# Kernel tuning notes

Measured on AMD Instinct MI355X. Metric: run time of the kernel, lower is better.

Reference implementation:

```python
import jax, jax.numpy as jnp
import numpy as np

SENTINEL = 1 << 20  # fill value for padded unique rows; far outside real coord range


def setup_inputs() -> dict:
    key = jax.random.key(0)
    k1, k2, k3, k4, k5, kw = jax.random.split(key, 6)
    M, C = 400000, 128
    voxel_features = jax.random.normal(k1, (M, C), dtype=jnp.float32)
    # coords: (batch_idx, z, y, x)
    b = jax.random.randint(k2, (M, 1), 0, 4, dtype=jnp.int32)
    z = jax.random.randint(k3, (M, 1), 0, 40, dtype=jnp.int32)
    y = jax.random.randint(k4, (M, 1), 0, 1024, dtype=jnp.int32)
    x = jax.random.randint(k5, (M, 1), 0, 1024, dtype=jnp.int32)
    voxel_coords = jnp.concatenate([b, z, y, x], axis=1)
    # layer-1 (stride=1) uses a random (in,out) matmul weight in the original;
    # materialize it as a fixed parameter for determinism.
    W0 = jax.random.normal(kw, (C, C), dtype=jnp.float32)
    return {"voxel_features": voxel_features, "voxel_coords": voxel_coords,
            "W0": W0, "batch_size": 4}


def _forward(voxel_features, W0, voxel_coords):
    M = voxel_features.shape[0]
    # layer 1: stride=1 -> relu then matmul (placeholder dense path)
    feats = jnp.maximum(voxel_features, 0.0) @ W0  # (M, 128)
    coords = voxel_coords
    # layers 2 and 3: stride=2 -> quantize coords (ALL 4 cols, incl. batch idx,
    # matching the original), unique, scatter-add features, relu
    for _ in range(2):
        coords = jnp.floor(coords.astype(jnp.float32) / 2.0).astype(jnp.int32)
        uniq, inv = jnp.unique(coords, axis=0, return_inverse=True,
                               size=M, fill_value=SENTINEL)
        inv = inv.reshape(-1)
        feats = jax.ops.segment_sum(feats, inv, num_segments=M)  # fused scatter-add
        feats = jnp.maximum(feats, 0.0)
        coords = uniq
    # rows beyond the true unique count are zero padding (sentinel coords)
    return feats


def reference(voxel_features, voxel_coords, W0, batch_size):
    return _forward(voxel_features, W0, voxel_coords)
```

## Files before the change

### kernel.cpp

```cpp
#include <hip/hip_runtime.h>
#include <stdint.h>

#define C 128

typedef __attribute__((ext_vector_type(8))) short bf16x8;
typedef __attribute__((ext_vector_type(4))) float f32x4;

__device__ __forceinline__ uint32_t f2bf1(float f) {
    uint32_t u = __float_as_uint(f);
    return (u + 0x7FFFu + ((u >> 16) & 1u)) >> 16;
}


__global__ __launch_bounds__(512) void zeroconv_kernel(
    uint4* __restrict__ zbase, int nquads,
    const float* __restrict__ W, ushort* __restrict__ Wt, int nzb) {
    int b = blockIdx.x, t = threadIdx.x;
    if (b < nzb) {
        int i = b * 512 + t;
        if (i < nquads) zbase[i] = (uint4){0u, 0u, 0u, 0u};
    } else {
        int id = (b - nzb) * 512 + t;
        int n = id >> 7, k = id & 127;
        Wt[id] = (ushort)f2bf1(W[k * C + n]);
    }
}

__global__ __launch_bounds__(512) void mark_kernel(
    const int* __restrict__ coords, uint32_t* __restrict__ bm1,
    uint32_t* __restrict__ bm2, int M) {
    int i = blockIdx.x * 512 + threadIdx.x;
    if (i >= M) return;
    int bb = coords[4*i+0], z = coords[4*i+1], y = coords[4*i+2], x = coords[4*i+3];
    uint32_t k1 = ((uint32_t)(bb>>1)<<23) | ((uint32_t)(z>>1)<<18) |
                  ((uint32_t)(y>>1)<<9)  | (uint32_t)(x>>1);
    uint32_t k2 = ((uint32_t)(z>>2)<<16) | ((uint32_t)(y>>2)<<8) | (uint32_t)(x>>2);
    atomicOr(&bm1[k1>>5], 1u << (k1 & 31));
    atomicOr(&bm2[k2>>5], 1u << (k2 & 31));
}

__device__ __forceinline__ void bscan1_512(const uint32_t* bm, uint32_t* bs,
                                           int blk, uint32_t* s, int t) {
    int base = blk * 1024 + t * 2;
    uint32_t sum = __popc(bm[base]) + __popc(bm[base+1]);
    s[t] = sum;
    __syncthreads();
    for (int off = 256; off > 0; off >>= 1) {
        if (t < off) s[t] += s[t + off];
        __syncthreads();
    }
    if (t == 0) bs[blk] = s[0];
}

__device__ __forceinline__ void bscan3_512(const uint32_t* bm, const uint32_t* bs,
                                           uint32_t* wp, int blk, uint32_t* s, int t) {
    int base = blk * 1024 + t * 2;
    uint32_t p0 = __popc(bm[base]), p1 = __popc(bm[base+1]);
    uint32_t sum = p0 + p1;
    s[t] = sum;
    __syncthreads();
    for (int off = 1; off < 512; off <<= 1) {
        uint32_t add = (t >= off) ? s[t - off] : 0u;
        __syncthreads();
        s[t] += add;
        __syncthreads();
    }
    uint32_t ex = s[t] - sum + bs[blk];
    wp[base]   = ex;
    wp[base+1] = ex + p0;
}

__device__ __forceinline__ void blksum_scan_512(uint32_t* bs, uint32_t* total,
                                                int nb, uint32_t* s, int t) {
    uint32_t v = (t < nb) ? bs[t] : 0u;
    s[t] = v;
    __syncthreads();
    for (int off = 1; off < 512; off <<= 1) {
        uint32_t add = (t >= off) ? s[t - off] : 0u;
        __syncthreads();
        s[t] += add;
        __syncthreads();
    }
    if (t < nb) bs[t] = s[t] - v;
    if (t == nb - 1) *total = s[t];
}

__device__ __forceinline__ void vscan1_512(const uint32_t* v, uint32_t* bs,
                                           int blk, int n, uint32_t* s, int t) {
    int base = blk * 1024 + t * 2;
    uint32_t sum = 0;
    if (base     < n) sum += v[base];
    if (base + 1 < n) sum += v[base+1];
    s[t] = sum;
    __syncthreads();
    for (int off = 256; off > 0; off >>= 1) {
        if (t < off) s[t] += s[t + off];
        __syncthreads();
    }
    if (t == 0) bs[blk] = s[0];
}

__device__ __forceinline__ void vscan3_512(const uint32_t* v, const uint32_t* bs,
                                           uint32_t* ex_out, int blk, int n,
                                           uint32_t* s, int t) {
    int base = blk * 1024 + t * 2;
    uint32_t p0 = (base     < n) ? v[base]   : 0u;
    uint32_t p1 = (base + 1 < n) ? v[base+1] : 0u;
    uint32_t sum = p0 + p1;
    s[t] = sum;
    __syncthreads();
    for (int off = 1; off < 512; off <<= 1) {
        uint32_t add = (t >= off) ? s[t - off] : 0u;
        __syncthreads();
        s[t] += add;
        __syncthreads();
    }
    uint32_t e = s[t] - sum + bs[blk];
    if (base     < n) ex_out[base]   = e;
    if (base + 1 < n) ex_out[base+1] = e + p0;
}

__global__ __launch_bounds__(512) void mscan1_kernel(
    const uint32_t* __restrict__ bm1, uint32_t* __restrict__ bs1,
    const uint32_t* __restrict__ bm2, uint32_t* __restrict__ bs2) {
    __shared__ uint32_t s[512];
    int b = blockIdx.x, t = threadIdx.x;
    if (b < 512) bscan1_512(bm1, bs1, b, s, t);
    else         bscan1_512(bm2, bs2, b - 512, s, t);
}

__global__ __launch_bounds__(512) void mscan2_kernel(
    uint32_t* __restrict__ bs1, uint32_t* __restrict__ bs2,
    uint32_t* __restrict__ totals) {
    __shared__ uint32_t s[512];
    int t = threadIdx.x;
    if (blockIdx.x == 0) blksum_scan_512(bs1, &totals[0], 512, s, t);
    else                 blksum_scan_512(bs2, &totals[1], 32,  s, t);
}

__global__ __launch_bounds__(512) void mscan3_kernel(
    const uint32_t* __restrict__ bm1, const uint32_t* __restrict__ bs1,
    uint32_t* __restrict__ wp1,
    const uint32_t* __restrict__ bm2, const uint32_t* __restrict__ bs2,
    uint32_t* __restrict__ wp2) {
    __shared__ uint32_t s[512];
    int b = blockIdx.x, t = threadIdx.x;
    if (b < 512) bscan3_512(bm1, bs1, wp1, b, s, t);
    else         bscan3_512(bm2, bs2, wp2, b - 512, s, t);
}

__global__ __launch_bounds__(512) void count_kernel(
    const int* __restrict__ coords, const uint32_t* __restrict__ bm1,
    const uint32_t* __restrict__ wp1, uint32_t* __restrict__ counts,
    uint32_t* __restrict__ rank1_arr, uint32_t* __restrict__ slot1, int M) {
    int i = blockIdx.x * 512 + threadIdx.x;
    if (i >= M) return;
    int b = coords[4*i+0], z = coords[4*i+1], y = coords[4*i+2], x = coords[4*i+3];
    uint32_t k1 = ((uint32_t)(b>>1)<<23) | ((uint32_t)(z>>1)<<18) |
                  ((uint32_t)(y>>1)<<9)  | (uint32_t)(x>>1);
    uint32_t r1 = wp1[k1>>5] + __popc(bm1[k1>>5] & ((1u << (k1 & 31)) - 1u));
    rank1_arr[i] = r1;
    slot1[i] = atomicAdd(&counts[r1], 1u);
}

__global__ __launch_bounds__(512) void mk1_kernel(
    const uint32_t* __restrict__ counts, uint32_t* __restrict__ bsc,
    const uint32_t* __restrict__ bm1, const uint32_t* __restrict__ wp1,
    const uint32_t* __restrict__ bm2, const uint32_t* __restrict__ wp2,
    uint32_t* __restrict__ parent_r2, uint32_t* __restrict__ rowcounts2,
    uint32_t* __restrict__ childbase, int M, int nbc, int nwords) {
    int b = blockIdx.x, t = threadIdx.x;
    if (b < nbc) {
        __shared__ uint32_t s[512];
        vscan1_512(counts, bsc, b, M, s, t);
        return;
    }
    int w = (b - nbc) * 512 + t;
    if (w >= nwords) return;
    uint32_t bits = bm1[w];
    if (!bits) return;
    uint32_t r1 = wp1[w];
    while (bits) {
        int bit = __ffs(bits) - 1;
        uint32_t k1 = ((uint32_t)w << 5) | (uint32_t)bit;
        uint32_t z1 = (k1 >> 18) & 31u, y1 = (k1 >> 9) & 511u, x1 = k1 & 511u;
        uint32_t k2 = ((z1 >> 1) << 16) | ((y1 >> 1) << 8) | (x1 >> 1);
        uint32_t word2 = bm2[k2 >> 5];
        uint32_t r2 = wp2[k2 >> 5] + __popc(word2 & ((1u << (k2 & 31)) - 1u));
        parent_r2[r1] = r2;
        childbase[r1] = atomicAdd(&rowcounts2[r2], counts[r1]);
        r1++;
        bits &= bits - 1;
    }
}

__global__ __launch_bounds__(512) void mk2_kernel(
    uint32_t* __restrict__ bsc, uint32_t* __restrict__ totals,
    const uint32_t* __restrict__ rowcounts2, uint32_t* __restrict__ bsc2,
    int M, int nbc) {
    __shared__ uint32_t s[512];
    int b = blockIdx.x, t = threadIdx.x;
    if (b == 0) blksum_scan_512(bsc, &totals[2], nbc, s, t);
    else        vscan1_512(rowcounts2, bsc2, b - 1, M, s, t);
}

__global__ __launch_bounds__(512) void mk3_kernel(
    const uint32_t* __restrict__ counts, const uint32_t* __restrict__ bsc,
    uint32_t* __restrict__ start1,
    uint32_t* __restrict__ bsc2, uint32_t* __restrict__ totals,
    int M, int nbc) {
    __shared__ uint32_t s[512];
    int b = blockIdx.x, t = threadIdx.x;
    if (b < nbc) vscan3_512(counts, bsc, start1, b, M, s, t);
    else         blksum_scan_512(bsc2, &totals[3], nbc, s, t);
}

__global__ __launch_bounds__(512) void mk4_kernel(
    const uint32_t* __restrict__ rank1_arr, const uint32_t* __restrict__ start1,
    const uint32_t* __restrict__ slot1, uint32_t* __restrict__ perm,
    const uint32_t* __restrict__ rowcounts2, const uint32_t* __restrict__ bsc2,
    uint32_t* __restrict__ rowstart2, int M, int npb, int nbc) {
    int b = blockIdx.x, t = threadIdx.x;
    if (b < npb) {
        int i = b * 512 + t;
        if (i >= M) return;
        uint32_t r1 = rank1_arr[i];
        perm[start1[r1] + slot1[i]] = i;
        return;
    }
    __shared__ uint32_t s[512];
    vscan3_512(rowcounts2, bsc2, rowstart2, b - npb, M, s, t);
}

__global__ __launch_bounds__(512) void flatten_kernel(
    const uint32_t* __restrict__ parent_r2, const uint32_t* __restrict__ counts,
    const uint32_t* __restrict__ start1, const uint32_t* __restrict__ rowstart2,
    const uint32_t* __restrict__ childbase, const uint32_t* __restrict__ perm,
    uint32_t* __restrict__ perm_f, const uint32_t* __restrict__ totals, int M) {
    int i = blockIdx.x * 512 + threadIdx.x;
    if (i >= M) return;
    uint32_t U1 = totals[0];
    if ((uint32_t)i >= U1) return;
    uint32_t r2 = parent_r2[i];
    uint32_t cnt = counts[i];
    uint32_t dst = rowstart2[r2] + childbase[i];
    uint32_t s = start1[i];
    perm_f[dst] = perm[s] | 0x80000000u;
    for (uint32_t q = 1; q < cnt; ++q) perm_f[dst + q] = perm[s + q];
}

__device__ __forceinline__ void gemm_loadX(const float* __restrict__ X,
                                           int tile, int lm, int kg, float4* pf) {
    const char* xb = (const char*)X + ((size_t)tile*16 + lm)*512 + kg*32;
    #pragma unroll
    for (int ks = 0; ks < 4; ++ks) {
        pf[2*ks]   = *(const float4*)(xb + ks*128);
        pf[2*ks+1] = *(const float4*)(xb + ks*128 + 16);
    }
}

__device__ __forceinline__ void gemm_compute(const float4* pf, const char* wbase,
                                             ushort* __restrict__ g, int tile,
                                             int lm, int kg) {
    bf16x8 af[4];
    #pragma unroll
    for (int ks = 0; ks < 4; ++ks) {
        float4 a = pf[2*ks], b = pf[2*ks+1];
        union { uint32_t u[4]; bf16x8 v; } cv;
        cv.u[0] = f2bf1(fmaxf(a.x,0.f)) | (f2bf1(fmaxf(a.y,0.f)) << 16);
        cv.u[1] = f2bf1(fmaxf(a.z,0.f)) | (f2bf1(fmaxf(a.w,0.f)) << 16);
        cv.u[2] = f2bf1(fmaxf(b.x,0.f)) | (f2bf1(fmaxf(b.y,0.f)) << 16);
        cv.u[3] = f2bf1(fmaxf(b.z,0.f)) | (f2bf1(fmaxf(b.w,0.f)) << 16);
        af[ks] = cv.v;
    }
    ushort* grow = g + (size_t)((size_t)tile*16 + 4*kg)*128 + lm;
    #pragma unroll
    for (int n = 0; n < 8; ++n) {
        bf16x8 b0 = *(const bf16x8*)(wbase + n*256);
        bf16x8 b1 = *(const bf16x8*)(wbase + n*256 + 8192);
        bf16x8 b2 = *(const bf16x8*)(wbase + n*256 + 16384);
        bf16x8 b3 = *(const bf16x8*)(wbase + n*256 + 24576);
        f32x4 acc = (f32x4){0.f, 0.f, 0.f, 0.f};
        acc = __builtin_amdgcn_mfma_f32_16x16x32_bf16(af[0], b0, acc, 0, 0, 0);
        acc = __builtin_amdgcn_mfma_f32_16x16x32_bf16(af[1], b1, acc, 0, 0, 0);
        acc = __builtin_amdgcn_mfma_f32_16x16x32_bf16(af[2], b2, acc, 0, 0, 0);
        acc = __builtin_amdgcn_mfma_f32_16x16x32_bf16(af[3], b3, acc, 0, 0, 0);
        #pragma unroll
        for (int r = 0; r < 4; ++r)
            grow[(size_t)r*128 + 16*n] = (ushort)f2bf1(acc[r]);
    }
}

__global__ __launch_bounds__(256) void gemm_kernel(
    const float* __restrict__ X, const ushort* __restrict__ Wt,
    ushort* __restrict__ g, int M) {
    __shared__ __align__(16) ushort wlds[16384];
    const int t = threadIdx.x;
    {
        int sm = t & 15, kc = t >> 4;
        const char* src = (const char*)Wt;
        char* dst = (char*)wlds;
        #pragma unroll
        for (int n = 0; n < 8; ++n) {
            uint4 v = *(const uint4*)(src + n*4096 + sm*256 + kc*16);
            *(uint4*)(dst + (kc>>2)*8192 + (kc&3)*2048 + n*256 + sm*16) = v;
        }
    }
    __syncthreads();
    const int l = t & 63;
    const int lm = l & 15, kg = l >> 4;
    const int ntiles = M >> 4;
    const int nw = gridDim.x * 4;
    int tile = blockIdx.x * 4 + (t >> 6);
    const char* wbase = (const char*)wlds + kg*2048 + lm*16;

    float4 pfA[8], pfB[8];
    if (tile < ntiles)      gemm_loadX(X, tile, lm, kg, pfA);
    if (tile + nw < ntiles) gemm_loadX(X, tile + nw, lm, kg, pfB);
    while (true) {
        if (tile >= ntiles) break;
        gemm_compute(pfA, wbase, g, tile, lm, kg);
        if (tile + 2*nw < ntiles) gemm_loadX(X, tile + 2*nw, lm, kg, pfA);
        tile += nw;
        if (tile >= ntiles) break;
        gemm_compute(pfB, wbase, g, tile, lm, kg);
        if (tile + 2*nw < ntiles) gemm_loadX(X, tile + 2*nw, lm, kg, pfB);
        tile += nw;
    }
}

__global__ __launch_bounds__(256) void gather2_kernel(
    const uint32_t* __restrict__ rowstart2, const uint32_t* __restrict__ rowcounts2,
    const uint32_t* __restrict__ perm_f, const ushort* __restrict__ g,
    float* __restrict__ out, int M) {
    int wid = (blockIdx.x * 256 + threadIdx.x) >> 6;
    wid = __builtin_amdgcn_readfirstlane(wid);
    int lane = threadIdx.x & 63;
    if (wid >= M) return;
    const uint32_t* G = (const uint32_t*)g;
    float accx = 0.f, accy = 0.f;
    uint32_t n = rowcounts2[wid];
    if (n) {
        uint32_t s = rowstart2[wid];
        uint32_t ev = (lane < (int)n) ? perm_f[s + lane] : 0u;
        float sx = 0.f, sy = 0.f;
        uint32_t ecur = (uint32_t)__shfl((int)ev, 0);
        uint32_t pk = G[(size_t)(ecur & 0x7FFFFFFFu) * 64 + lane];
        for (uint32_t q = 1; q < n; ++q) {
            uint32_t en = (q < 64u) ? (uint32_t)__shfl((int)ev, (int)q)
                                    : perm_f[s + q];
            uint32_t pkn = G[(size_t)(en & 0x7FFFFFFFu) * 64 + lane];
            sx += __uint_as_float(pk << 16);
            sy += __uint_as_float(pk & 0xFFFF0000u);
            if (en >> 31) {
                accx += fmaxf(sx, 0.f); accy += fmaxf(sy, 0.f);
                sx = 0.f; sy = 0.f;
            }
            pk = pkn;
        }
        sx += __uint_as_float(pk << 16);
        sy += __uint_as_float(pk & 0xFFFF0000u);
        accx += fmaxf(sx, 0.f);
        accy += fmaxf(sy, 0.f);
    }
    float2 o; o.x = accx; o.y = accy;
    ((float2*)out)[(size_t)wid * 64 + lane] = o;
}

extern "C" void kernel_launch(void* const* d_in, const int* in_sizes, int n_in,
                              void* d_out, int out_size, void* d_ws, size_t ws_size,
                              hipStream_t stream) {
    const float* X      = (const float*)d_in[0];
    const int*   coords = (const int*)d_in[1];
    const float* W      = (const float*)d_in[2];
    const int M = in_sizes[0] / C;

    const int NW1 = 1 << 19;
    const int NW2 = 1 << 15;
    const int NBC = (M + 1023) / 1024;
    const int NPB = (M + 511) / 512;

    char* ws = (char*)d_ws;
    size_t off = 0;
    ushort*   g         = (ushort*)(ws + off);   off += (size_t)M * C * 2;
    uint32_t* bm1       = (uint32_t*)(ws + off); off += (size_t)NW1 * 4;
    uint32_t* bm2       = (uint32_t*)(ws + off); off += (size_t)NW2 * 4;
    uint32_t* counts    = (uint32_t*)(ws + off); off += (size_t)M * 4;
    uint32_t* rowcounts2= (uint32_t*)(ws + off); off += (size_t)M * 4;
    const size_t zero_off   = (size_t)M * C * 2;
    const size_t zero_bytes = off - zero_off;
    uint32_t* wp1       = (uint32_t*)(ws + off); off += (size_t)NW1 * 4;
    uint32_t* wp2       = (uint32_t*)(ws + off); off += (size_t)NW2 * 4;
    uint32_t* bs1       = (uint32_t*)(ws + off); off += 512 * 4;
    uint32_t* bs2       = (uint32_t*)(ws + off); off += 512 * 4;
    uint32_t* bsc       = (uint32_t*)(ws + off); off += 512 * 4;
    uint32_t* bsc2      = (uint32_t*)(ws + off); off += 512 * 4;
    uint32_t* totals    = (uint32_t*)(ws + off); off += 4 * 4;
    uint32_t* start1    = (uint32_t*)(ws + off); off += (size_t)M * 4;
    uint32_t* rank1_arr = (uint32_t*)(ws + off); off += (size_t)M * 4;
    uint32_t* slot1     = (uint32_t*)(ws + off); off += (size_t)M * 4;
    uint32_t* perm      = (uint32_t*)(ws + off); off += (size_t)M * 4;
    uint32_t* parent_r2 = (uint32_t*)(ws + off); off += (size_t)M * 4;
    uint32_t* childbase = (uint32_t*)(ws + off); off += (size_t)M * 4;
    uint32_t* rowstart2 = (uint32_t*)(ws + off); off += (size_t)M * 4;
    ushort*   Wt        = (ushort*)(ws + off);   off += (size_t)C * C * 2;
    uint32_t* perm_f    = rank1_arr;

    const int NQ  = (int)(zero_bytes / 16);
    const int NZB = (NQ + 511) / 512;

    zeroconv_kernel<<<NZB + 32, 512, 0, stream>>>((uint4*)(ws + zero_off), NQ, W, Wt, NZB);
    mark_kernel<<<NPB, 512, 0, stream>>>(coords, bm1, bm2, M);
    mscan1_kernel<<<544, 512, 0, stream>>>(bm1, bs1, bm2, bs2);
    mscan2_kernel<<<2, 512, 0, stream>>>(bs1, bs2, totals);
    mscan3_kernel<<<544, 512, 0, stream>>>(bm1, bs1, wp1, bm2, bs2, wp2);
    count_kernel<<<NPB, 512, 0, stream>>>(coords, bm1, wp1, counts, rank1_arr, slot1, M);
    mk1_kernel<<<NBC + NW1/512, 512, 0, stream>>>(counts, bsc, bm1, wp1, bm2, wp2,
                                                  parent_r2, rowcounts2, childbase,
                                                  M, NBC, NW1);
    mk2_kernel<<<1 + NBC, 512, 0, stream>>>(bsc, totals, rowcounts2, bsc2, M, NBC);
    mk3_kernel<<<NBC + 1, 512, 0, stream>>>(counts, bsc, start1, bsc2, totals, M, NBC);
    mk4_kernel<<<NPB + NBC, 512, 0, stream>>>(rank1_arr, start1, slot1, perm,
                                              rowcounts2, bsc2, rowstart2, M, NPB, NBC);
    flatten_kernel<<<NPB, 512, 0, stream>>>(
        parent_r2, counts, start1, rowstart2, childbase, perm, perm_f, totals, M);
    gemm_kernel<<<1280, 256, 0, stream>>>(X, Wt, g, M);
    gather2_kernel<<<(M + 3) / 4, 256, 0, stream>>>(
        rowstart2, rowcounts2, perm_f, g, (float*)d_out, M);
}
```

Measured before the change: 278.7 us.

## Split dense GEMM into slices fused into each index-building kernel

Removes the standalone GEMM launch and hands contiguous tile ranges of the relu+bf16 MFMA matmul to extra blocks appended to each of the latency-bound index-building kernels (mark, scans, count, mk1-4, flatten). The small serial kernels then share the GPU with GEMM work instead of leaving it mostly idle. Several scan kernels move to 256-thread blocks handling four words per thread, and the final output uses nontemporal stores. In exchange every kernel now reserves 32KB of shared memory, which can lower occupancy for the index-building blocks, and the GEMM slice percentages are hand-tuned.

```diff
diff --git a/kernel.cpp b/kernel.cpp
--- a/kernel.cpp
+++ b/kernel.cpp
@@ -5,6 +5,7 @@
 
 typedef __attribute__((ext_vector_type(8))) short bf16x8;
 typedef __attribute__((ext_vector_type(4))) float f32x4;
+typedef __attribute__((ext_vector_type(2))) float f32x2;
 
 __device__ __forceinline__ uint32_t f2bf1(float f) {
     uint32_t u = __float_as_uint(f);
@@ -12,54 +13,103 @@
 }
 
 
-__global__ __launch_bounds__(512) void zeroconv_kernel(
-    uint4* __restrict__ zbase, int nquads,
-    const float* __restrict__ W, ushort* __restrict__ Wt, int nzb) {
-    int b = blockIdx.x, t = threadIdx.x;
-    if (b < nzb) {
-        int i = b * 512 + t;
-        if (i < nquads) zbase[i] = (uint4){0u, 0u, 0u, 0u};
-    } else {
-        int id = (b - nzb) * 512 + t;
-        int n = id >> 7, k = id & 127;
-        Wt[id] = (ushort)f2bf1(W[k * C + n]);
-    }
-}
-
-__global__ __launch_bounds__(512) void mark_kernel(
-    const int* __restrict__ coords, uint32_t* __restrict__ bm1,
-    uint32_t* __restrict__ bm2, int M) {
-    int i = blockIdx.x * 512 + threadIdx.x;
-    if (i >= M) return;
-    int bb = coords[4*i+0], z = coords[4*i+1], y = coords[4*i+2], x = coords[4*i+3];
-    uint32_t k1 = ((uint32_t)(bb>>1)<<23) | ((uint32_t)(z>>1)<<18) |
-                  ((uint32_t)(y>>1)<<9)  | (uint32_t)(x>>1);
-    uint32_t k2 = ((uint32_t)(z>>2)<<16) | ((uint32_t)(y>>2)<<8) | (uint32_t)(x>>2);
-    atomicOr(&bm1[k1>>5], 1u << (k1 & 31));
-    atomicOr(&bm2[k2>>5], 1u << (k2 & 31));
-}
-
-__device__ __forceinline__ void bscan1_512(const uint32_t* bm, uint32_t* bs,
+__device__ __forceinline__ void gemm_loadX(const float* __restrict__ X,
+                                           int tile, int lm, int kg, float4* pf) {
+    const char* xb = (const char*)X + ((size_t)tile*16 + lm)*512 + kg*32;
+    #pragma unroll
+    for (int ks = 0; ks < 4; ++ks) {
+        pf[2*ks]   = *(const float4*)(xb + ks*128);
+        pf[2*ks+1] = *(const float4*)(xb + ks*128 + 16);
+    }
+}
+
+__device__ __forceinline__ void gemm_compute(const float4* pf, const char* wbase,
+                                             ushort* __restrict__ g, int tile,
+                                             int lm, int kg) {
+    bf16x8 af[4];
+    #pragma unroll
+    for (int ks = 0; ks < 4; ++ks) {
+        float4 a = pf[2*ks], b = pf[2*ks+1];
+        union { uint32_t u[4]; bf16x8 v; } cv;
+        cv.u[0] = f2bf1(fmaxf(a.x,0.f)) | (f2bf1(fmaxf(a.y,0.f)) << 16);
+        cv.u[1] = f2bf1(fmaxf(a.z,0.f)) | (f2bf1(fmaxf(a.w,0.f)) << 16);
+        cv.u[2] = f2bf1(fmaxf(b.x,0.f)) | (f2bf1(fmaxf(b.y,0.f)) << 16);
+        cv.u[3] = f2bf1(fmaxf(b.z,0.f)) | (f2bf1(fmaxf(b.w,0.f)) << 16);
+        af[ks] = cv.v;
+    }
+    ushort* grow = g + (size_t)((size_t)tile*16 + 4*kg)*128 + lm;
+    #pragma unroll
+    for (int n = 0; n < 8; ++n) {
+        bf16x8 b0 = *(const bf16x8*)(wbase + n*256);
+        bf16x8 b1 = *(const bf16x8*)(wbase + n*256 + 8192);
+        bf16x8 b2 = *(const bf16x8*)(wbase + n*256 + 16384);
+        bf16x8 b3 = *(const bf16x8*)(wbase + n*256 + 24576);
+        f32x4 acc = (f32x4){0.f, 0.f, 0.f, 0.f};
+        acc = __builtin_amdgcn_mfma_f32_16x16x32_bf16(af[0], b0, acc, 0, 0, 0);
+        acc = __builtin_amdgcn_mfma_f32_16x16x32_bf16(af[1], b1, acc, 0, 0, 0);
+        acc = __builtin_amdgcn_mfma_f32_16x16x32_bf16(af[2], b2, acc, 0, 0, 0);
+        acc = __builtin_amdgcn_mfma_f32_16x16x32_bf16(af[3], b3, acc, 0, 0, 0);
+        #pragma unroll
+        for (int r = 0; r < 4; ++r)
+            grow[(size_t)r*128 + 16*n] = (ushort)f2bf1(acc[r]);
+    }
+}
+
+__device__ void gemm_slice(const float* __restrict__ X,
+                           const ushort* __restrict__ Wt,
+                           ushort* __restrict__ g, char* smem,
+                           int gb, int ngb, int t0, int t1) {
+    const int t = threadIdx.x;
+    const int nthreads = blockDim.x;
+    for (int q = t; q < 2048; q += nthreads) {
+        int ks = q >> 9, kg = (q >> 7) & 3, n = (q >> 4) & 7, sm = q & 15;
+        ((uint4*)smem)[q] = ((const uint4*)Wt)[n*256 + sm*16 + ks*4 + kg];
+    }
+    __syncthreads();
+    const int l = t & 63, wv = t >> 6, nwv = nthreads >> 6;
+    const int lm = l & 15, kg = l >> 4;
+    const char* wbase = smem + kg*2048 + lm*16;
+    const int stride = ngb * nwv;
+    int tile = t0 + gb * nwv + wv;
+
+    float4 pfA[8], pfB[8];
+    if (tile < t1)          gemm_loadX(X, tile, lm, kg, pfA);
+    if (tile + stride < t1) gemm_loadX(X, tile + stride, lm, kg, pfB);
+    while (true) {
+        if (tile >= t1) break;
+        gemm_compute(pfA, wbase, g, tile, lm, kg);
+        if (tile + 2*stride < t1) gemm_loadX(X, tile + 2*stride, lm, kg, pfA);
+        tile += stride;
+        if (tile >= t1) break;
+        gemm_compute(pfB, wbase, g, tile, lm, kg);
+        if (tile + 2*stride < t1) gemm_loadX(X, tile + 2*stride, lm, kg, pfB);
+        tile += stride;
+    }
+}
+
+__device__ __forceinline__ void bscan1_256(const uint32_t* bm, uint32_t* bs,
                                            int blk, uint32_t* s, int t) {
-    int base = blk * 1024 + t * 2;
-    uint32_t sum = __popc(bm[base]) + __popc(bm[base+1]);
+    int base = blk * 1024 + t * 4;
+    uint32_t sum = __popc(bm[base]) + __popc(bm[base+1]) +
+                   __popc(bm[base+2]) + __popc(bm[base+3]);
     s[t] = sum;
     __syncthreads();
-    for (int off = 256; off > 0; off >>= 1) {
+    for (int off = 128; off > 0; off >>= 1) {
         if (t < off) s[t] += s[t + off];
         __syncthreads();
     }
     if (t == 0) bs[blk] = s[0];
 }
 
-__device__ __forceinline__ void bscan3_512(const uint32_t* bm, const uint32_t* bs,
+__device__ __forceinline__ void bscan3_256(const uint32_t* bm, const uint32_t* bs,
                                            uint32_t* wp, int blk, uint32_t* s, int t) {
-    int base = blk * 1024 + t * 2;
-    uint32_t p0 = __popc(bm[base]), p1 = __popc(bm[base+1]);
-    uint32_t sum = p0 + p1;
+    int base = blk * 1024 + t * 4;
+    uint32_t p0 = __popc(bm[base]),   p1 = __popc(bm[base+1]);
+    uint32_t p2 = __popc(bm[base+2]), p3 = __popc(bm[base+3]);
+    uint32_t sum = p0 + p1 + p2 + p3;
     s[t] = sum;
     __syncthreads();
-    for (int off = 1; off < 512; off <<= 1) {
+    for (int off = 1; off < 256; off <<= 1) {
         uint32_t add = (t >= off) ? s[t - off] : 0u;
         __syncthreads();
         s[t] += add;
@@ -68,6 +118,23 @@
     uint32_t ex = s[t] - sum + bs[blk];
     wp[base]   = ex;
     wp[base+1] = ex + p0;
+    wp[base+2] = ex + p0 + p1;
+    wp[base+3] = ex + p0 + p1 + p2;
+}
+
+__device__ __forceinline__ void vscan1_256(const uint32_t* v, uint32_t* bs,
+                                           int blk, int n, uint32_t* s, int t) {
+    int base = blk * 1024 + t * 4;
+    uint32_t sum = 0;
+    #pragma unroll
+    for (int j = 0; j < 4; j++) sum += (base + j < n) ? v[base + j] : 0u;
+    s[t] = sum;
+    __syncthreads();
+    for (int off = 128; off > 0; off >>= 1) {
+        if (t < off) s[t] += s[t + off];
+        __syncthreads();
+    }
+    if (t == 0) bs[blk] = s[0];
 }
 
 __device__ __forceinline__ void blksum_scan_512(uint32_t* bs, uint32_t* total,
@@ -120,62 +187,114 @@
     if (base + 1 < n) ex_out[base+1] = e + p0;
 }
 
-__global__ __launch_bounds__(512) void mscan1_kernel(
+__global__ __launch_bounds__(256) void zeroconv_kernel(
+    uint4* __restrict__ zbase, int nquads,
+    const float* __restrict__ W, ushort* __restrict__ Wt, int nzb) {
+    int b = blockIdx.x, t = threadIdx.x;
+    if (b < nzb) {
+        int i = b * 256 + t;
+        if (i < nquads) zbase[i] = (uint4){0u, 0u, 0u, 0u};
+    } else {
+        int id = (b - nzb) * 256 + t;
+        int n = id >> 7, k = id & 127;
+        Wt[id] = (ushort)f2bf1(W[k * C + n]);
+    }
+}
+
+__global__ __launch_bounds__(256) void markg_kernel(
+    const int* __restrict__ coords, uint32_t* __restrict__ bm1,
+    uint32_t* __restrict__ bm2, int M, int nprep,
+    const float* __restrict__ X, const ushort* __restrict__ Wt,
+    ushort* __restrict__ g, int ngb, int t0, int t1) {
+    __shared__ __align__(16) char smem[32768];
+    int b = blockIdx.x;
+    if (b >= nprep) { gemm_slice(X, Wt, g, smem, b - nprep, ngb, t0, t1); return; }
+    int i = b * 256 + threadIdx.x;
+    if (i >= M) return;
+    int bb = coords[4*i+0], z = coords[4*i+1], y = coords[4*i+2], x = coords[4*i+3];
+    uint32_t k1 = ((uint32_t)(bb>>1)<<23) | ((uint32_t)(z>>1)<<18) |
+                  ((uint32_t)(y>>1)<<9)  | (uint32_t)(x>>1);
+    uint32_t k2 = ((uint32_t)(z>>2)<<16) | ((uint32_t)(y>>2)<<8) | (uint32_t)(x>>2);
+    atomicOr(&bm1[k1>>5], 1u << (k1 & 31));
+    atomicOr(&bm2[k2>>5], 1u << (k2 & 31));
+}
+
+__global__ __launch_bounds__(256) void mscan1g_kernel(
     const uint32_t* __restrict__ bm1, uint32_t* __restrict__ bs1,
-    const uint32_t* __restrict__ bm2, uint32_t* __restrict__ bs2) {
-    __shared__ uint32_t s[512];
-    int b = blockIdx.x, t = threadIdx.x;
-    if (b < 512) bscan1_512(bm1, bs1, b, s, t);
-    else         bscan1_512(bm2, bs2, b - 512, s, t);
-}
-
-__global__ __launch_bounds__(512) void mscan2_kernel(
+    const uint32_t* __restrict__ bm2, uint32_t* __restrict__ bs2, int nprep,
+    const float* __restrict__ X, const ushort* __restrict__ Wt,
+    ushort* __restrict__ g, int ngb, int t0, int t1) {
+    __shared__ __align__(16) char smem[32768];
+    int b = blockIdx.x, t = threadIdx.x;
+    if (b >= nprep) { gemm_slice(X, Wt, g, smem, b - nprep, ngb, t0, t1); return; }
+    uint32_t* s = (uint32_t*)smem;
+    if (b < 512) bscan1_256(bm1, bs1, b, s, t);
+    else         bscan1_256(bm2, bs2, b - 512, s, t);
+}
+
+__global__ __launch_bounds__(512) void mscan2g_kernel(
     uint32_t* __restrict__ bs1, uint32_t* __restrict__ bs2,
-    uint32_t* __restrict__ totals) {
-    __shared__ uint32_t s[512];
-    int t = threadIdx.x;
-    if (blockIdx.x == 0) blksum_scan_512(bs1, &totals[0], 512, s, t);
-    else                 blksum_scan_512(bs2, &totals[1], 32,  s, t);
-}
-
-__global__ __launch_bounds__(512) void mscan3_kernel(
+    uint32_t* __restrict__ totals, int nprep,
+    const float* __restrict__ X, const ushort* __restrict__ Wt,
+    ushort* __restrict__ g, int ngb, int t0, int t1) {
+    __shared__ __align__(16) char smem[32768];
+    int b = blockIdx.x, t = threadIdx.x;
+    if (b >= nprep) { gemm_slice(X, Wt, g, smem, b - nprep, ngb, t0, t1); return; }
+    uint32_t* s = (uint32_t*)smem;
+    if (b == 0) blksum_scan_512(bs1, &totals[0], 512, s, t);
+    else        blksum_scan_512(bs2, &totals[1], 32,  s, t);
+}
+
+__global__ __launch_bounds__(256) void mscan3g_kernel(
     const uint32_t* __restrict__ bm1, const uint32_t* __restrict__ bs1,
     uint32_t* __restrict__ wp1,
     const uint32_t* __restrict__ bm2, const uint32_t* __restrict__ bs2,
-    uint32_t* __restrict__ wp2) {
-    __shared__ uint32_t s[512];
-    int b = blockIdx.x, t = threadIdx.x;
-    if (b < 512) bscan3_512(bm1, bs1, wp1, b, s, t);
-    else         bscan3_512(bm2, bs2, wp2, b - 512, s, t);
-}
-
-__global__ __launch_bounds__(512) void count_kernel(
+    uint32_t* __restrict__ wp2, int nprep,
+    const float* __restrict__ X, const ushort* __restrict__ Wt,
+    ushort* __restrict__ g, int ngb, int t0, int t1) {
+    __shared__ __align__(16) char smem[32768];
+    int b = blockIdx.x, t = threadIdx.x;
+    if (b >= nprep) { gemm_slice(X, Wt, g, smem, b - nprep, ngb, t0, t1); return; }
+    uint32_t* s = (uint32_t*)smem;
+    if (b < 512) bscan3_256(bm1, bs1, wp1, b, s, t);
+    else         bscan3_256(bm2, bs2, wp2, b - 512, s, t);
+}
+
+__global__ __launch_bounds__(256) void countg_kernel(
     const int* __restrict__ coords, const uint32_t* __restrict__ bm1,
     const uint32_t* __restrict__ wp1, uint32_t* __restrict__ counts,
-    uint32_t* __restrict__ rank1_arr, uint32_t* __restrict__ slot1, int M) {
-    int i = blockIdx.x * 512 + threadIdx.x;
+    uint32_t* __restrict__ rank1_arr, uint32_t* __restrict__ slot1, int M, int nprep,
+    const float* __restrict__ X, const ushort* __restrict__ Wt,
+    ushort* __restrict__ g, int ngb, int t0, int t1) {
+    __shared__ __align__(16) char smem[32768];
+    int b = blockIdx.x;
+    if (b >= nprep) { gemm_slice(X, Wt, g, smem, b - nprep, ngb, t0, t1); return; }
+    int i = b * 256 + threadIdx.x;
     if (i >= M) return;
-    int b = coords[4*i+0], z = coords[4*i+1], y = coords[4*i+2], x = coords[4*i+3];
-    uint32_t k1 = ((uint32_t)(b>>1)<<23) | ((uint32_t)(z>>1)<<18) |
+    int bb = coords[4*i+0], z = coords[4*i+1], y = coords[4*i+2], x = coords[4*i+3];
+    uint32_t k1 = ((uint32_t)(bb>>1)<<23) | ((uint32_t)(z>>1)<<18) |
                   ((uint32_t)(y>>1)<<9)  | (uint32_t)(x>>1);
     uint32_t r1 = wp1[k1>>5] + __popc(bm1[k1>>5] & ((1u << (k1 & 31)) - 1u));
     rank1_arr[i] = r1;
     slot1[i] = atomicAdd(&counts[r1], 1u);
 }
 
-__global__ __launch_bounds__(512) void mk1_kernel(
+__global__ __launch_bounds__(256) void mk1g_kernel(
     const uint32_t* __restrict__ counts, uint32_t* __restrict__ bsc,
     const uint32_t* __restrict__ bm1, const uint32_t* __restrict__ wp1,
     const uint32_t* __restrict__ bm2, const uint32_t* __restrict__ wp2,
     uint32_t* __restrict__ parent_r2, uint32_t* __restrict__ rowcounts2,
-    uint32_t* __restrict__ childbase, int M, int nbc, int nwords) {
-    int b = blockIdx.x, t = threadIdx.x;
+    uint32_t* __restrict__ childbase, int M, int nbc, int nwords, int nprep,
+    const float* __restrict__ X, const ushort* __restrict__ Wt,
+    ushort* __restrict__ g, int ngb, int t0, int t1) {
+    __shared__ __align__(16) char smem[32768];
+    int b = blockIdx.x, t = threadIdx.x;
+    if (b >= nprep) { gemm_slice(X, Wt, g, smem, b - nprep, ngb, t0, t1); return; }
     if (b < nbc) {
-        __shared__ uint32_t s[512];
-        vscan1_512(counts, bsc, b, M, s, t);
+        vscan1_256(counts, bsc, b, M, (uint32_t*)smem, t);
         return;
     }
-    int w = (b - nbc) * 512 + t;
+    int w = (b - nbc) * 256 + t;
     if (w >= nwords) return;
     uint32_t bits = bm1[w];
     if (!bits) return;
@@ -194,33 +313,45 @@
     }
 }
 
-__global__ __launch_bounds__(512) void mk2_kernel(
+__global__ __launch_bounds__(512) void mk2g_kernel(
     uint32_t* __restrict__ bsc, uint32_t* __restrict__ totals,
     const uint32_t* __restrict__ rowcounts2, uint32_t* __restrict__ bsc2,
-    int M, int nbc) {
-    __shared__ uint32_t s[512];
-    int b = blockIdx.x, t = threadIdx.x;
+    int M, int nbc, int nprep,
+    const float* __restrict__ X, const ushort* __restrict__ Wt,
+    ushort* __restrict__ g, int ngb, int t0, int t1) {
+    __shared__ __align__(16) char smem[32768];
+    int b = blockIdx.x, t = threadIdx.x;
+    if (b >= nprep) { gemm_slice(X, Wt, g, smem, b - nprep, ngb, t0, t1); return; }
+    uint32_t* s = (uint32_t*)smem;
     if (b == 0) blksum_scan_512(bsc, &totals[2], nbc, s, t);
     else        vscan1_512(rowcounts2, bsc2, b - 1, M, s, t);
 }
 
-__global__ __launch_bounds__(512) void mk3_kernel(
+__global__ __launch_bounds__(512) void mk3g_kernel(
     const uint32_t* __restrict__ counts, const uint32_t* __restrict__ bsc,
     uint32_t* __restrict__ start1,
     uint32_t* __restrict__ bsc2, uint32_t* __restrict__ totals,
-    int M, int nbc) {
-    __shared__ uint32_t s[512];
-    int b = blockIdx.x, t = threadIdx.x;
+    int M, int nbc, int nprep,
+    const float* __restrict__ X, const ushort* __restrict__ Wt,
+    ushort* __restrict__ g, int ngb, int t0, int t1) {
+    __shared__ __align__(16) char smem[32768];
+    int b = blockIdx.x, t = threadIdx.x;
+    if (b >= nprep) { gemm_slice(X, Wt, g, smem, b - nprep, ngb, t0, t1); return; }
+    uint32_t* s = (uint32_t*)smem;
     if (b < nbc) vscan3_512(counts, bsc, start1, b, M, s, t);
     else         blksum_scan_512(bsc2, &totals[3], nbc, s, t);
 }
 
-__global__ __launch_bounds__(512) void mk4_kernel(
+__global__ __launch_bounds__(512) void mk4g_kernel(
     const uint32_t* __restrict__ rank1_arr, const uint32_t* __restrict__ start1,
     const uint32_t* __restrict__ slot1, uint32_t* __restrict__ perm,
     const uint32_t* __restrict__ rowcounts2, const uint32_t* __restrict__ bsc2,
-    uint32_t* __restrict__ rowstart2, int M, int npb, int nbc) {
-    int b = blockIdx.x, t = threadIdx.x;
+    uint32_t* __restrict__ rowstart2, int M, int npb, int nbc, int nprep,
+    const float* __restrict__ X, const ushort* __restrict__ Wt,
+    ushort* __restrict__ g, int ngb, int t0, int t1) {
+    __shared__ __align__(16) char smem[32768];
+    int b = blockIdx.x, t = threadIdx.x;
+    if (b >= nprep) { gemm_slice(X, Wt, g, smem, b - nprep, ngb, t0, t1); return; }
     if (b < npb) {
         int i = b * 512 + t;
         if (i >= M) return;
@@ -228,16 +359,21 @@
         perm[start1[r1] + slot1[i]] = i;
         return;
     }
-    __shared__ uint32_t s[512];
-    vscan3_512(rowcounts2, bsc2, rowstart2, b - npb, M, s, t);
-}
-
-__global__ __launch_bounds__(512) void flatten_kernel(
+    vscan3_512(rowcounts2, bsc2, rowstart2, b - npb, M, (uint32_t*)smem, t);
+}
+
+__global__ __launch_bounds__(512) void flatteng_kernel(
     const uint32_t* __restrict__ parent_r2, const uint32_t* __restrict__ counts,
     const uint32_t* __restrict__ start1, const uint32_t* __restrict__ rowstart2,
     const uint32_t* __restrict__ childbase, const uint32_t* __restrict__ perm,
-    uint32_t* __restrict__ perm_f, const uint32_t* __restrict__ totals, int M) {
-    int i = blockIdx.x * 512 + threadIdx.x;
+    uint32_t* __restrict__ perm_f, const uint32_t* __restrict__ totals, int M,
+    int nprep,
+    const float* __restrict__ X, const ushort* __restrict__ Wt,
+    ushort* __restrict__ g, int ngb, int t0, int t1) {
+    __shared__ __align__(16) char smem[32768];
+    int b = blockIdx.x;
+    if (b >= nprep) { gemm_slice(X, Wt, g, smem, b - nprep, ngb, t0, t1); return; }
+    int i = b * 512 + threadIdx.x;
     if (i >= M) return;
     uint32_t U1 = totals[0];
     if ((uint32_t)i >= U1) return;
@@ -247,86 +383,6 @@
     uint32_t s = start1[i];
     perm_f[dst] = perm[s] | 0x80000000u;
     for (uint32_t q = 1; q < cnt; ++q) perm_f[dst + q] = perm[s + q];
-}
-
-__device__ __forceinline__ void gemm_loadX(const float* __restrict__ X,
-                                           int tile, int lm, int kg, float4* pf) {
-    const char* xb = (const char*)X + ((size_t)tile*16 + lm)*512 + kg*32;
-    #pragma unroll
-    for (int ks = 0; ks < 4; ++ks) {
-        pf[2*ks]   = *(const float4*)(xb + ks*128);
-        pf[2*ks+1] = *(const float4*)(xb + ks*128 + 16);
-    }
-}
-
-__device__ __forceinline__ void gemm_compute(const float4* pf, const char* wbase,
-                                             ushort* __restrict__ g, int tile,
-                                             int lm, int kg) {
-    bf16x8 af[4];
-    #pragma unroll
-    for (int ks = 0; ks < 4; ++ks) {
-        float4 a = pf[2*ks], b = pf[2*ks+1];
-        union { uint32_t u[4]; bf16x8 v; } cv;
-        cv.u[0] = f2bf1(fmaxf(a.x,0.f)) | (f2bf1(fmaxf(a.y,0.f)) << 16);
-        cv.u[1] = f2bf1(fmaxf(a.z,0.f)) | (f2bf1(fmaxf(a.w,0.f)) << 16);
-        cv.u[2] = f2bf1(fmaxf(b.x,0.f)) | (f2bf1(fmaxf(b.y,0.f)) << 16);
-        cv.u[3] = f2bf1(fmaxf(b.z,0.f)) | (f2bf1(fmaxf(b.w,0.f)) << 16);
-        af[ks] = cv.v;
-    }
-    ushort* grow = g + (size_t)((size_t)tile*16 + 4*kg)*128 + lm;
-    #pragma unroll
-    for (int n = 0; n < 8; ++n) {
-        bf16x8 b0 = *(const bf16x8*)(wbase + n*256);
-        bf16x8 b1 = *(const bf16x8*)(wbase + n*256 + 8192);
-        bf16x8 b2 = *(const bf16x8*)(wbase + n*256 + 16384);
-        bf16x8 b3 = *(const bf16x8*)(wbase + n*256 + 24576);
-        f32x4 acc = (f32x4){0.f, 0.f, 0.f, 0.f};
-        acc = __builtin_amdgcn_mfma_f32_16x16x32_bf16(af[0], b0, acc, 0, 0, 0);
-        acc = __builtin_amdgcn_mfma_f32_16x16x32_bf16(af[1], b1, acc, 0, 0, 0);
-        acc = __builtin_amdgcn_mfma_f32_16x16x32_bf16(af[2], b2, acc, 0, 0, 0);
-        acc = __builtin_amdgcn_mfma_f32_16x16x32_bf16(af[3], b3, acc, 0, 0, 0);
-        #pragma unroll
-        for (int r = 0; r < 4; ++r)
-            grow[(size_t)r*128 + 16*n] = (ushort)f2bf1(acc[r]);
-    }
-}
-
-__global__ __launch_bounds__(256) void gemm_kernel(
-    const float* __restrict__ X, const ushort* __restrict__ Wt,
-    ushort* __restrict__ g, int M) {
-    __shared__ __align__(16) ushort wlds[16384];
-    const int t = threadIdx.x;
-    {
-        int sm = t & 15, kc = t >> 4;
-        const char* src = (const char*)Wt;
-        char* dst = (char*)wlds;
-        #pragma unroll
-        for (int n = 0; n < 8; ++n) {
-            uint4 v = *(const uint4*)(src + n*4096 + sm*256 + kc*16);
-            *(uint4*)(dst + (kc>>2)*8192 + (kc&3)*2048 + n*256 + sm*16) = v;
-        }
-    }
-    __syncthreads();
-    const int l = t & 63;
-    const int lm = l & 15, kg = l >> 4;
-    const int ntiles = M >> 4;
-    const int nw = gridDim.x * 4;
-    int tile = blockIdx.x * 4 + (t >> 6);
-    const char* wbase = (const char*)wlds + kg*2048 + lm*16;
-
-    float4 pfA[8], pfB[8];
-    if (tile < ntiles)      gemm_loadX(X, tile, lm, kg, pfA);
-    if (tile + nw < ntiles) gemm_loadX(X, tile + nw, lm, kg, pfB);
-    while (true) {
-        if (tile >= ntiles) break;
-        gemm_compute(pfA, wbase, g, tile, lm, kg);
-        if (tile + 2*nw < ntiles) gemm_loadX(X, tile + 2*nw, lm, kg, pfA);
-        tile += nw;
-        if (tile >= ntiles) break;
-        gemm_compute(pfB, wbase, g, tile, lm, kg);
-        if (tile + 2*nw < ntiles) gemm_loadX(X, tile + 2*nw, lm, kg, pfB);
-        tile += nw;
-    }
 }
 
 __global__ __launch_bounds__(256) void gather2_kernel(
@@ -363,8 +419,8 @@
         accx += fmaxf(sx, 0.f);
         accy += fmaxf(sy, 0.f);
     }
-    float2 o; o.x = accx; o.y = accy;
-    ((float2*)out)[(size_t)wid * 64 + lane] = o;
+    f32x2 o; o[0] = accx; o[1] = accy;
+    __builtin_nontemporal_store(o, (f32x2*)out + (size_t)wid * 64 + lane);
 }
 
 extern "C" void kernel_launch(void* const* d_in, const int* in_sizes, int n_in,
@@ -378,7 +434,8 @@
     const int NW1 = 1 << 19;
     const int NW2 = 1 << 15;
     const int NBC = (M + 1023) / 1024;
-    const int NPB = (M + 511) / 512;
+    const int NPB256 = (M + 255) / 256;
+    const int NPB512 = (M + 511) / 512;
 
     char* ws = (char*)d_ws;
     size_t off = 0;
@@ -407,24 +464,42 @@
     uint32_t* perm_f    = rank1_arr;
 
     const int NQ  = (int)(zero_bytes / 16);
-    const int NZB = (NQ + 511) / 512;
-
-    zeroconv_kernel<<<NZB + 32, 512, 0, stream>>>((uint4*)(ws + zero_off), NQ, W, Wt, NZB);
-    mark_kernel<<<NPB, 512, 0, stream>>>(coords, bm1, bm2, M);
-    mscan1_kernel<<<544, 512, 0, stream>>>(bm1, bs1, bm2, bs2);
-    mscan2_kernel<<<2, 512, 0, stream>>>(bs1, bs2, totals);
-    mscan3_kernel<<<544, 512, 0, stream>>>(bm1, bs1, wp1, bm2, bs2, wp2);
-    count_kernel<<<NPB, 512, 0, stream>>>(coords, bm1, wp1, counts, rank1_arr, slot1, M);
-    mk1_kernel<<<NBC + NW1/512, 512, 0, stream>>>(counts, bsc, bm1, wp1, bm2, wp2,
-                                                  parent_r2, rowcounts2, childbase,
-                                                  M, NBC, NW1);
-    mk2_kernel<<<1 + NBC, 512, 0, stream>>>(bsc, totals, rowcounts2, bsc2, M, NBC);
-    mk3_kernel<<<NBC + 1, 512, 0, stream>>>(counts, bsc, start1, bsc2, totals, M, NBC);
-    mk4_kernel<<<NPB + NBC, 512, 0, stream>>>(rank1_arr, start1, slot1, perm,
-                                              rowcounts2, bsc2, rowstart2, M, NPB, NBC);
-    flatten_kernel<<<NPB, 512, 0, stream>>>(
-        parent_r2, counts, start1, rowstart2, childbase, perm, perm_f, totals, M);
-    gemm_kernel<<<1280, 256, 0, stream>>>(X, Wt, g, M);
+    const int NZB = (NQ + 255) / 256;
+
+    const int NT = M >> 4;
+    auto cut = [&](int pct) { return (int)((long long)NT * pct / 100); };
+    const int c1 = cut(12), c2 = cut(21), c3 = cut(25), c4 = cut(34),
+              c5 = cut(46), c6 = cut(59), c7 = cut(63), c8 = cut(67),
+              c9 = cut(80);
+    const int NG256 = 500, NG512 = 250;
+
+    zeroconv_kernel<<<NZB + 64, 256, 0, stream>>>((uint4*)(ws + zero_off), NQ, W, Wt, NZB);
+    markg_kernel<<<NPB256 + NG256, 256, 0, stream>>>(coords, bm1, bm2, M, NPB256,
+                                                     X, Wt, g, NG256, 0, c1);
+    mscan1g_kernel<<<544 + NG256, 256, 0, stream>>>(bm1, bs1, bm2, bs2, 544,
+                                                    X, Wt, g, NG256, c1, c2);
+    mscan2g_kernel<<<2 + NG512, 512, 0, stream>>>(bs1, bs2, totals, 2,
+                                                  X, Wt, g, NG512, c2, c3);
+    mscan3g_kernel<<<544 + NG256, 256, 0, stream>>>(bm1, bs1, wp1, bm2, bs2, wp2, 544,
+                                                    X, Wt, g, NG256, c3, c4);
+    countg_kernel<<<NPB256 + NG256, 256, 0, stream>>>(coords, bm1, wp1, counts,
+                                                      rank1_arr, slot1, M, NPB256,
+                                                      X, Wt, g, NG256, c4, c5);
+    mk1g_kernel<<<NBC + NW1/256 + NG256, 256, 0, stream>>>(
+        counts, bsc, bm1, wp1, bm2, wp2, parent_r2, rowcounts2, childbase,
+        M, NBC, NW1, NBC + NW1/256, X, Wt, g, NG256, c5, c6);
+    mk2g_kernel<<<1 + NBC + NG512, 512, 0, stream>>>(bsc, totals, rowcounts2, bsc2,
+                                                     M, NBC, 1 + NBC,
+                                                     X, Wt, g, NG512, c6, c7);
+    mk3g_kernel<<<NBC + 1 + NG512, 512, 0, stream>>>(counts, bsc, start1, bsc2, totals,
+                                                     M, NBC, NBC + 1,
+                                                     X, Wt, g, NG512, c7, c8);
+    mk4g_kernel<<<NPB512 + NBC + NG512, 512, 0, stream>>>(
+        rank1_arr, start1, slot1, perm, rowcounts2, bsc2, rowstart2,
+        M, NPB512, NBC, NPB512 + NBC, X, Wt, g, NG512, c8, c9);
+    flatteng_kernel<<<NPB512 + NG512, 512, 0, stream>>>(
+        parent_r2, counts, start1, rowstart2, childbase, perm, perm_f, totals, M,
+        NPB512, X, Wt, g, NG512, c9, NT);
     gather2_kernel<<<(M + 3) / 4, 256, 0, stream>>>(
         rowstart2, rowcounts2, perm_f, g, (float*)d_out, M);
 }
```

After: 407.5 us. +46.2%, slower.
